# Optimization experiments

Hardware: AMD Instinct MI355X
Metric: run time of the kernel (lower is better)

The kernel has to match this reference:

```python
import jax, jax.numpy as jnp
import numpy as np

H = 256  # GRU hidden size
V = 56   # decoder vocab / fc1 out


def gru_cell(x, h, wih, whh, bih, bhh):
    # PyTorch GRU cell math (gate order: r, z, n)
    gi = x @ wih.T + bih
    gh = h @ whh.T + bhh
    ir, iz, inn = jnp.split(gi, 3, axis=-1)
    hr, hz, hn = jnp.split(gh, 3, axis=-1)
    r = jax.nn.sigmoid(ir + hr)
    z = jax.nn.sigmoid(iz + hz)
    n = jnp.tanh(inn + r * hn)
    return (1.0 - z) * n + z * h


def gru_scan(seq, h0, wih, whh, bih, bhh):
    def step(h, xt):
        h = gru_cell(xt, h, wih, whh, bih, bhh)
        return h, h
    hT, ys = jax.lax.scan(step, h0, seq)
    return ys, hT


def bigru(seq, pf, pb):
    # seq: (S, N, F). Returns (S, N, 2H), final fwd hidden (N,H), final bwd hidden (N,H)
    S, N, _ = seq.shape
    h0 = jnp.zeros((N, H), seq.dtype)
    yf, hf = gru_scan(seq, h0, *pf)
    yb_rev, hb = gru_scan(seq[::-1], h0, *pb)
    return jnp.concatenate([yf, yb_rev[::-1]], axis=-1), hf, hb


def setup_inputs() -> dict:
    key = jax.random.key(0)
    ks = iter(jax.random.split(key, 32))
    s = 0.05
    p = {}
    p["x"] = jax.random.normal(next(ks), (64, 48, 512, 2, 2), dtype=jnp.float32)
    # bi_gru_1: input 192
    for d in ("f", "b"):
        p[f"w_ih_1{d}"] = jax.random.normal(next(ks), (3 * H, 192), jnp.float32) * s
        p[f"w_hh_1{d}"] = jax.random.normal(next(ks), (3 * H, H), jnp.float32) * s
        p[f"b_ih_1{d}"] = jax.random.normal(next(ks), (3 * H,), jnp.float32) * s
        p[f"b_hh_1{d}"] = jax.random.normal(next(ks), (3 * H,), jnp.float32) * s
    # bi_gru_2: input 512
    for d in ("f", "b"):
        p[f"w_ih_2{d}"] = jax.random.normal(next(ks), (3 * H, 2 * H), jnp.float32) * s
        p[f"w_hh_2{d}"] = jax.random.normal(next(ks), (3 * H, H), jnp.float32) * s
        p[f"b_ih_2{d}"] = jax.random.normal(next(ks), (3 * H,), jnp.float32) * s
        p[f"b_hh_2{d}"] = jax.random.normal(next(ks), (3 * H,), jnp.float32) * s
    # decoder GRU: input 56
    p["w_ih_d"] = jax.random.normal(next(ks), (3 * H, V), jnp.float32) * s
    p["w_hh_d"] = jax.random.normal(next(ks), (3 * H, H), jnp.float32) * s
    p["b_ih_d"] = jax.random.normal(next(ks), (3 * H,), jnp.float32) * s
    p["b_hh_d"] = jax.random.normal(next(ks), (3 * H,), jnp.float32) * s
    p["w_fc1"] = jax.random.normal(next(ks), (V, H), jnp.float32) * s
    p["b_fc1"] = jax.random.normal(next(ks), (V,), jnp.float32) * s
    p["w_adj"] = jax.random.normal(next(ks), (H, 2 * H), jnp.float32) * s
    p["b_adj"] = jax.random.normal(next(ks), (H,), jnp.float32) * s
    p["target_length"] = 6
    return p


def reference(x,
              w_ih_1f, w_hh_1f, b_ih_1f, b_hh_1f,
              w_ih_1b, w_hh_1b, b_ih_1b, b_hh_1b,
              w_ih_2f, w_hh_2f, b_ih_2f, b_hh_2f,
              w_ih_2b, w_hh_2b, b_ih_2b, b_hh_2b,
              w_ih_d, w_hh_d, b_ih_d, b_hh_d,
              w_fc1, b_fc1, w_adj, b_adj,
              target_length):
    B, C, T, Hh, Ww = x.shape
    # permute(2,0,1,3,4).contiguous().view(B, T, -1): flat buffer in (T,B,..) order reshaped to (B,T,feat)
    seq = jnp.transpose(x, (2, 0, 1, 3, 4)).reshape(B, T, C * Hh * Ww)
    # GRUs run seq-first: seq dim = B, batch dim = T (faithful to the torch code)
    y1, _, _ = bigru(seq, (w_ih_1f, w_hh_1f, b_ih_1f, b_hh_1f),
                     (w_ih_1b, w_hh_1b, b_ih_1b, b_hh_1b))
    # dropout is identity at inference
    y2, hf, hb = bigru(y1, (w_ih_2f, w_hh_2f, b_ih_2f, b_hh_2f),
                       (w_ih_2b, w_hh_2b, b_ih_2b, b_hh_2b))
    combined = jnp.concatenate([hf, hb], axis=-1)       # (T, 2H)
    dec_h_all = combined @ w_adj.T + b_adj              # (T, H)
    dec_h = dec_h_all[:B]                               # loop over b in range(B) selects first B rows
    inp0 = jnp.zeros((B, V), x.dtype)

    def step(carry, _):
        inp, h = carry
        h = gru_cell(inp, h, w_ih_d, w_hh_d, b_ih_d, b_hh_d)
        out = h @ w_fc1.T + b_fc1
        return (out, h), out

    _, outs = jax.lax.scan(step, (inp0, dec_h), None, length=target_length)
    return jnp.transpose(outs, (1, 0, 2))  # (B, target_length, V)
```

## Files before the change

kernel.cpp:

```cpp
#include <hip/hip_runtime.h>
#include <hip/hip_fp16.h>
#include <stdint.h>


#define HD 256
#define G3 768
#define NSEQ 64
#define NSTEP 64

typedef _Float16 hvec2 __attribute__((ext_vector_type(2)));
typedef _Float16 f16x8 __attribute__((ext_vector_type(8)));
typedef float f32x4 __attribute__((ext_vector_type(4)));

__device__ __forceinline__ float sigmf(float x) {
    return 1.0f / (1.0f + __expf(-x));
}

#if __has_builtin(__builtin_amdgcn_fdot2)
__device__ __forceinline__ float fdot2u(uint32_t w, uint32_t h, float acc) {
    return __builtin_amdgcn_fdot2(__builtin_bit_cast(hvec2, w),
                                  __builtin_bit_cast(hvec2, h), acc, false);
}
#else
__device__ __forceinline__ float fdot2u(uint32_t w, uint32_t h, float acc) {
    const __half2 wv = __builtin_bit_cast(__half2, w);
    const __half2 hv = __builtin_bit_cast(__half2, h);
    acc += __half2float(wv.x) * __half2float(hv.x);
    acc += __half2float(wv.y) * __half2float(hv.y);
    return acc;
}
#endif

__device__ __forceinline__ uint32_t pkh(float a, float b) {
    uint32_t lo = __half_as_ushort(__float2half_rn(a));
    uint32_t hi = __half_as_ushort(__float2half_rn(b));
    return lo | (hi << 16);
}

#define L16(X) X(0) X(1) X(2) X(3) X(4) X(5) X(6) X(7) \
  X(8) X(9) X(10) X(11) X(12) X(13) X(14) X(15)

#define LRES(i) \
    const uint4 wr##i = wbase[(i) * G3]; \
    const uint4 wz##i = wbase[(i) * G3 + 256]; \
    const uint4 wn##i = wbase[(i) * G3 + 512];

#define DRES(i) { \
    const uint4 hp = *(const uint4*)&hb[hoff + 4 * (i)]; \
    ar0 = fdot2u(wr##i.x, hp.x, ar0); ar1 = fdot2u(wr##i.y, hp.y, ar1); \
    ar0 = fdot2u(wr##i.z, hp.z, ar0); ar1 = fdot2u(wr##i.w, hp.w, ar1); \
    az0 = fdot2u(wz##i.x, hp.x, az0); az1 = fdot2u(wz##i.y, hp.y, az1); \
    az0 = fdot2u(wz##i.z, hp.z, az0); az1 = fdot2u(wz##i.w, hp.w, az1); \
    an0 = fdot2u(wn##i.x, hp.x, an0); an1 = fdot2u(wn##i.y, hp.y, an1); \
    an0 = fdot2u(wn##i.z, hp.z, an0); an1 = fdot2u(wn##i.w, hp.w, an1); }

__global__ __launch_bounds__(256) void prep_all(
    const float* __restrict__ whh1f, const float* __restrict__ whh1b,
    const float* __restrict__ whh2f, const float* __restrict__ whh2b,
    const float* __restrict__ whhd,
    uint32_t* __restrict__ wt1f, uint32_t* __restrict__ wt1b,
    uint32_t* __restrict__ wt2f, uint32_t* __restrict__ wt2b,
    uint32_t* __restrict__ wtd,
    const float* __restrict__ wih1f, const float* __restrict__ wih1b,
    const float* __restrict__ wih2f, const float* __restrict__ wih2b,
    __half* __restrict__ wih1f_h, __half* __restrict__ wih1b_h,
    __half* __restrict__ wih2f_h, __half* __restrict__ wih2b_h,
    const float* __restrict__ wihd, const float* __restrict__ wadj,
    const float* __restrict__ wfc1,
    float* __restrict__ wihdT, float* __restrict__ wadjT,
    float* __restrict__ wfc1T,
    const float* __restrict__ x, __half* __restrict__ seqg)
{
    const int b   = blockIdx.x;
    const int tid = threadIdx.x;

    if (b < 480) {
        const int y = b / 96;
        const float* w; uint32_t* o;
        switch (y) {
            case 0: w = whh1f; o = wt1f; break;
            case 1: w = whh1b; o = wt1b; break;
            case 2: w = whh2f; o = wt2f; break;
            case 3: w = whh2b; o = wt2b; break;
            default: w = whhd; o = wtd; break;
        }
        const int idx = (b % 96) * 256 + tid;
        const int j = idx >> 5, q = idx & 31;
        const float4 fa = *(const float4*)(w + j * HD + 8 * q);
        const float4 fb = *(const float4*)(w + j * HD + 8 * q + 4);
        uint4 r;
        r.x = pkh(fa.x, fa.y); r.y = pkh(fa.z, fa.w);
        r.z = pkh(fb.x, fb.y); r.w = pkh(fb.z, fb.w);
        ((uint4*)o)[q * G3 + j] = r;
    } else if (b < 1536) {
        const float* s; __half* d; int i4;
        if (b < 624)       { s = wih1f; d = wih1f_h; i4 = (b - 480) * 256 + tid; }
        else if (b < 768)  { s = wih1b; d = wih1b_h; i4 = (b - 624) * 256 + tid; }
        else if (b < 1152) { s = wih2f; d = wih2f_h; i4 = (b - 768) * 256 + tid; }
        else               { s = wih2b; d = wih2b_h; i4 = (b - 1152) * 256 + tid; }
        const float4 v = *(const float4*)(s + (size_t)i4 * 4);
        __half2 lo; lo.x = __float2half_rn(v.x); lo.y = __float2half_rn(v.y);
        __half2 hi; hi.x = __float2half_rn(v.z); hi.y = __float2half_rn(v.w);
        *(__half2*)(d + (size_t)i4 * 4)     = lo;
        *(__half2*)(d + (size_t)i4 * 4 + 2) = hi;
    } else if (b < 2272) {
        const int idx = (b - 1536) * 256 + tid;
        if (idx < 43008) {
            int v = idx / G3, j = idx % G3;
            wihdT[idx] = wihd[j * 56 + v];
        } else if (idx < 43008 + 131072) {
            int i2 = idx - 43008;
            int f = i2 / HD, i = i2 % HD;
            wadjT[i2] = wadj[i * 512 + f];
        } else {
            int i3 = idx - 174080;
            int k = i3 / 56, v = i3 % 56;
            wfc1T[i3] = wfc1[v * HD + k];
        }
    } else {
        const int idx = (b - 2272) * 256 + tid;
        const int f = idx % 192;
        const int m = idx / 192;
        const int n = m >> 6, s = m & 63;
        seqg[idx] = __float2half(
            x[n * 98304 + (f >> 2) * 2048 + s * 32 + (f & 3)]);
    }
}

template <int K>
__global__ __launch_bounds__(256) void gemm_mfma(
    const __half* __restrict__ A,
    const __half* __restrict__ B0, const __half* __restrict__ B1,
    const float* __restrict__ bias0, const float* __restrict__ bias1,
    float* __restrict__ C0, float* __restrict__ C1)
{
    const __half* B    = blockIdx.z ? B1 : B0;
    const float*  bias = blockIdx.z ? bias1 : bias0;
    float*        C    = blockIdx.z ? C1 : C0;
    const int m0 = blockIdx.x * 64;
    const int n0 = blockIdx.y * 64;
    const int w  = threadIdx.x >> 6;
    const int l  = threadIdx.x & 63;
    const int lr = l & 15;
    const int lk = (l >> 4) * 8;

    const __half* arow = A + (size_t)(m0 + w * 16 + lr) * K + lk;
    const __half* brow = B + (size_t)(n0 + lr) * K + lk;

    f32x4 acc0 = {0.f, 0.f, 0.f, 0.f};
    f32x4 acc1 = acc0, acc2 = acc0, acc3 = acc0;

#pragma unroll
    for (int k0 = 0; k0 < K; k0 += 32) {
        const f16x8 a  = *(const f16x8*)(arow + k0);
        const f16x8 b0 = *(const f16x8*)(brow + k0);
        const f16x8 b1 = *(const f16x8*)(brow + 16 * K + k0);
        const f16x8 b2 = *(const f16x8*)(brow + 32 * K + k0);
        const f16x8 b3 = *(const f16x8*)(brow + 48 * K + k0);
        acc0 = __builtin_amdgcn_mfma_f32_16x16x32_f16(a, b0, acc0, 0, 0, 0);
        acc1 = __builtin_amdgcn_mfma_f32_16x16x32_f16(a, b1, acc1, 0, 0, 0);
        acc2 = __builtin_amdgcn_mfma_f32_16x16x32_f16(a, b2, acc2, 0, 0, 0);
        acc3 = __builtin_amdgcn_mfma_f32_16x16x32_f16(a, b3, acc3, 0, 0, 0);
    }

    const int crow = m0 + w * 16 + (l >> 4) * 4;
    const int ccol = n0 + lr;
    float* cp = C + (size_t)crow * G3 + ccol;
    const float bb0 = bias[ccol];
    const float bb1 = bias[ccol + 16];
    const float bb2 = bias[ccol + 32];
    const float bb3 = bias[ccol + 48];
#pragma unroll
    for (int j = 0; j < 4; ++j) {
        cp[(size_t)j * G3 +  0] = acc0[j] + bb0;
        cp[(size_t)j * G3 + 16] = acc1[j] + bb1;
        cp[(size_t)j * G3 + 32] = acc2[j] + bb2;
        cp[(size_t)j * G3 + 48] = acc3[j] + bb3;
    }
}

__global__ __launch_bounds__(512, 1) void gru_scan(
    const float* __restrict__ giF, const float* __restrict__ giB,
    const uint32_t* __restrict__ wTF, const uint32_t* __restrict__ wTB,
    const float* __restrict__ bhhF, const float* __restrict__ bhhB,
    __half* __restrict__ y1h, float* __restrict__ hfin)
{
    const int dir = blockIdx.x & 1;
    const int n   = blockIdx.x >> 1;
    const int t   = threadIdx.x;
    const int tr  = t & 255;
    const int kh  = t >> 8;
    const int hoff = kh * 64;
    const float* gi  = dir ? giB : giF;
    const float* bhh = dir ? bhhB : bhhF;
    const uint4* wbase = (const uint4*)(dir ? wTB : wTF)
                       + (size_t)(kh * 16) * G3 + tr;

    __shared__ __align__(16) uint32_t h1u[2][HD / 2];
    __shared__ float ph_r[HD], ph_z[HD], ph_n[HD];
    __shared__ float gin[2][G3];

    L16(LRES)
    const float bhr = bhh[tr], bhz = bhh[256 + tr], bhn = bhh[512 + tr];

    const float* gbase = gi + (size_t)n * NSTEP * G3;
    const int s0 = dir ? (NSTEP - 1) : 0;
#pragma unroll
    for (int i = t; i < G3; i += 512) gin[0][i] = gbase[s0 * G3 + i];

    float h_own = 0.0f;
    if (t < HD / 2) h1u[0][t] = 0u;
    __syncthreads();

    int s = s0;
    for (int step = 0; step < NSTEP; ++step) {
        const uint32_t* hb = h1u[step & 1];
        float ar0 = 0.f, ar1 = 0.f;
        float az0 = 0.f, az1 = 0.f;
        float an0 = 0.f, an1 = 0.f;
        L16(DRES)

        if (kh) {
            ph_r[tr] = ar0 + ar1;
            ph_z[tr] = az0 + az1;
            ph_n[tr] = an0 + an1;
        }
        __syncthreads();
        const int s_nxt = dir ? (step < NSTEP - 1 ? NSTEP - 2 - step : 0)
                              : (step < NSTEP - 1 ? step + 1 : NSTEP - 1);
        if (kh == 0) {
            const float* gcur = gin[step & 1];
            const float ghr = (ar0 + ar1) + ph_r[tr] + bhr;
            const float ghz = (az0 + az1) + ph_z[tr] + bhz;
            const float ghn = (an0 + an1) + ph_n[tr] + bhn;
            const float r  = sigmf(gcur[tr] + ghr);
            const float z  = sigmf(gcur[256 + tr] + ghz);
            const float nn = tanhf(gcur[512 + tr] + r * ghn);
            const float hnew = (1.0f - z) * nn + z * h_own;
            h_own = hnew;
            const __half hh = __float2half(hnew);
            ((__half*)h1u[(step + 1) & 1])[tr] = hh;
            y1h[(size_t)(n * NSTEP + s) * 512 + dir * HD + tr] = hh;
        } else {
            float* gnxt = gin[(step + 1) & 1];
            gnxt[tr]       = gbase[s_nxt * G3 + tr];
            gnxt[256 + tr] = gbase[s_nxt * G3 + 256 + tr];
            gnxt[512 + tr] = gbase[s_nxt * G3 + 512 + tr];
        }
        s = s_nxt;
        __syncthreads();
    }
    if (kh == 0)
        hfin[(size_t)(dir * NSEQ + n) * HD + tr] = h_own;
}

__global__ __launch_bounds__(768, 3) void decoder_kernel(
    const float* __restrict__ hfin, const float* __restrict__ wadjT,
    const float* __restrict__ badj, const uint32_t* __restrict__ wTd,
    const float* __restrict__ wihdT, const float* __restrict__ bihd,
    const float* __restrict__ bhhd, const float* __restrict__ wfc1T,
    const float* __restrict__ bfc1, float* __restrict__ out)
{
    const int n = blockIdx.x, t = threadIdx.x;
    const uint4* wq = (const uint4*)wTd + t;

    __shared__ __align__(16) uint32_t h1u[2][HD / 2];
    __shared__ float comb[512];
    __shared__ float ghs[G3], gis[G3];
    __shared__ float hfp[HD];
    __shared__ float inp[56];
    __shared__ float pf1[448];

    const float bi = bihd[t], bh = bhhd[t];

    if (t < 512)
        comb[t] = (t < 256) ? hfin[(size_t)n * HD + t]
                            : hfin[(size_t)(NSEQ + n) * HD + (t - 256)];
    if (t < 56) inp[t] = 0.0f;
    __syncthreads();

    float h_own = 0.0f;
    if (t < HD) {
        float acc = badj[t];
#pragma unroll 8
        for (int f = 0; f < 512; ++f) acc += wadjT[f * HD + t] * comb[f];
        h_own = acc;
        ((__half*)h1u[0])[t] = __float2half(acc);
        hfp[t] = acc;
    }
    __syncthreads();

    for (int step = 0; step < 6; ++step) {
        const uint32_t* hb = h1u[step & 1];
        float a0 = 0.f, a1 = 0.f;
#pragma unroll 8
        for (int q = 0; q < 32; ++q) {
            const uint4 w = wq[q * G3];
            const uint4 hp = *(const uint4*)&hb[4 * q];
            a0 = fdot2u(w.x, hp.x, a0); a1 = fdot2u(w.y, hp.y, a1);
            a0 = fdot2u(w.z, hp.z, a0); a1 = fdot2u(w.w, hp.w, a1);
        }
        float ai = bi;
#pragma unroll 8
        for (int v = 0; v < 56; ++v) ai += wihdT[v * G3 + t] * inp[v];
        ghs[t] = a0 + a1 + bh;
        gis[t] = ai;
        __syncthreads();
        if (t < HD) {
            const float r  = sigmf(gis[t] + ghs[t]);
            const float z  = sigmf(gis[HD + t] + ghs[HD + t]);
            const float nn = tanhf(gis[2 * HD + t] + r * ghs[2 * HD + t]);
            const float hnew = (1.0f - z) * nn + z * h_own;
            h_own = hnew;
            ((__half*)h1u[(step + 1) & 1])[t] = __float2half(hnew);
            hfp[t] = hnew;
        }
        __syncthreads();
        if (t < 448) {
            const int v = t >> 3, g = t & 7;
            float o = 0.f;
#pragma unroll
            for (int k2 = 0; k2 < 32; ++k2)
                o += wfc1T[(g * 32 + k2) * 56 + v] * hfp[g * 32 + k2];
            pf1[t] = o;
        }
        __syncthreads();
        if (t < 56) {
            float o = bfc1[t];
#pragma unroll
            for (int g = 0; g < 8; ++g) o += pf1[t * 8 + g];
            out[(size_t)n * 336 + step * 56 + t] = o;
            inp[t] = o;
        }
        __syncthreads();
    }
}

extern "C" void kernel_launch(void* const* d_in, const int* in_sizes, int n_in,
                              void* d_out, int out_size, void* d_ws, size_t ws_size,
                              hipStream_t stream)
{
    const float* x      = (const float*)d_in[0];
    const float* wih1f  = (const float*)d_in[1];
    const float* whh1f  = (const float*)d_in[2];
    const float* bih1f  = (const float*)d_in[3];
    const float* bhh1f  = (const float*)d_in[4];
    const float* wih1b  = (const float*)d_in[5];
    const float* whh1b  = (const float*)d_in[6];
    const float* bih1b  = (const float*)d_in[7];
    const float* bhh1b  = (const float*)d_in[8];
    const float* wih2f  = (const float*)d_in[9];
    const float* whh2f  = (const float*)d_in[10];
    const float* bih2f  = (const float*)d_in[11];
    const float* bhh2f  = (const float*)d_in[12];
    const float* wih2b  = (const float*)d_in[13];
    const float* whh2b  = (const float*)d_in[14];
    const float* bih2b  = (const float*)d_in[15];
    const float* bhh2b  = (const float*)d_in[16];
    const float* wihd   = (const float*)d_in[17];
    const float* whhd   = (const float*)d_in[18];
    const float* bihd   = (const float*)d_in[19];
    const float* bhhd   = (const float*)d_in[20];
    const float* wfc1   = (const float*)d_in[21];
    const float* bfc1   = (const float*)d_in[22];
    const float* wadj   = (const float*)d_in[23];
    const float* badj   = (const float*)d_in[24];

    float* ws = (float*)d_ws;
    __half*   seqg_h  = (__half*)(ws + 0);
    float*    gi_f    = ws + 393216;
    float*    gi_b    = ws + 3538944;
    __half*   y1h     = (__half*)(ws + 6684672);
    float*    hfin    = ws + 7733248;
    uint32_t* wt1f    = (uint32_t*)(ws + 7782400);
    uint32_t* wt1b    = (uint32_t*)(ws + 7880704);
    uint32_t* wt2f    = (uint32_t*)(ws + 7979008);
    uint32_t* wt2b    = (uint32_t*)(ws + 8077312);
    uint32_t* wtd     = (uint32_t*)(ws + 8175616);
    __half*   wih1f_h = (__half*)(ws + 8273920);
    __half*   wih1b_h = (__half*)(ws + 8347648);
    __half*   wih2f_h = (__half*)(ws + 8421376);
    __half*   wih2b_h = (__half*)(ws + 8617984);
    float*    wihdT   = ws + 8814592;
    float*    wadjT   = ws + 8857600;
    float*    wfc1T   = ws + 8988672;

    prep_all<<<5344, 256, 0, stream>>>(
        whh1f, whh1b, whh2f, whh2b, whhd,
        wt1f, wt1b, wt2f, wt2b, wtd,
        wih1f, wih1b, wih2f, wih2b,
        wih1f_h, wih1b_h, wih2f_h, wih2b_h,
        wihd, wadj, wfc1, wihdT, wadjT, wfc1T,
        x, seqg_h);

    gemm_mfma<192><<<dim3(64, 12, 2), 256, 0, stream>>>(
        seqg_h, wih1f_h, wih1b_h, bih1f, bih1b, gi_f, gi_b);
    gru_scan<<<128, 512, 0, stream>>>(
        gi_f, gi_b, wt1f, wt1b, bhh1f, bhh1b, y1h, hfin);

    gemm_mfma<512><<<dim3(64, 12, 2), 256, 0, stream>>>(
        y1h, wih2f_h, wih2b_h, bih2f, bih2b, gi_f, gi_b);
    gru_scan<<<128, 512, 0, stream>>>(
        gi_f, gi_b, wt2f, wt2b, bhh2f, bhh2b, y1h, hfin);

    decoder_kernel<<<64, 768, 0, stream>>>(
        hfin, wadjT, badj, wtd, wihdT, bihd, bhhd, wfc1T, bfc1,
        (float*)d_out);
}
```

Baseline: 345.6 us.

## Split GRU recurrent weights between registers and LDS; stage GEMM B tile in LDS

The scan kernel used to keep all 16 chunks of recurrent weights in registers per thread. It now keeps 10 chunks in registers and stages the other 6 in dynamic shared memory (about 147 KB), which lowers register pressure at the cost of LDS reads on every step. The input-projection GEMM now copies its 64-row B tile into padded shared memory before the MFMA loop, so B rows are no longer read repeatedly from global memory. Both changes add LDS traffic and a large LDS footprint per block.

Result: faster. 331.8 us (-4.0%).

```diff
diff --git a/kernel.cpp b/kernel.cpp
--- a/kernel.cpp
+++ b/kernel.cpp
@@ -7,6 +7,7 @@
 #define G3 768
 #define NSEQ 64
 #define NSTEP 64
+#define LSTG 6
 
 typedef _Float16 hvec2 __attribute__((ext_vector_type(2)));
 typedef _Float16 f16x8 __attribute__((ext_vector_type(8)));
@@ -37,8 +38,7 @@
     return lo | (hi << 16);
 }
 
-#define L16(X) X(0) X(1) X(2) X(3) X(4) X(5) X(6) X(7) \
-  X(8) X(9) X(10) X(11) X(12) X(13) X(14) X(15)
+#define L10(X) X(0) X(1) X(2) X(3) X(4) X(5) X(6) X(7) X(8) X(9)
 
 #define LRES(i) \
     const uint4 wr##i = wbase[(i) * G3]; \
@@ -134,6 +134,9 @@
     const float* __restrict__ bias0, const float* __restrict__ bias1,
     float* __restrict__ C0, float* __restrict__ C1)
 {
+    extern __shared__ __half Bs[];
+    constexpr int LDB = K + 8;
+
     const __half* B    = blockIdx.z ? B1 : B0;
     const float*  bias = blockIdx.z ? bias1 : bias0;
     float*        C    = blockIdx.z ? C1 : C0;
@@ -144,8 +147,16 @@
     const int lr = l & 15;
     const int lk = (l >> 4) * 8;
 
+    const __half* bsrc = B + (size_t)n0 * K;
+#pragma unroll
+    for (int i = threadIdx.x; i < 64 * K / 8; i += 256) {
+        const int r = i / (K / 8), g = i % (K / 8);
+        *(f16x8*)(Bs + r * LDB + g * 8) = *(const f16x8*)(bsrc + i * 8);
+    }
+    __syncthreads();
+
     const __half* arow = A + (size_t)(m0 + w * 16 + lr) * K + lk;
-    const __half* brow = B + (size_t)(n0 + lr) * K + lk;
+    const __half* brow = Bs + lr * LDB + lk;
 
     f32x4 acc0 = {0.f, 0.f, 0.f, 0.f};
     f32x4 acc1 = acc0, acc2 = acc0, acc3 = acc0;
@@ -154,9 +165,9 @@
     for (int k0 = 0; k0 < K; k0 += 32) {
         const f16x8 a  = *(const f16x8*)(arow + k0);
         const f16x8 b0 = *(const f16x8*)(brow + k0);
-        const f16x8 b1 = *(const f16x8*)(brow + 16 * K + k0);
-        const f16x8 b2 = *(const f16x8*)(brow + 32 * K + k0);
-        const f16x8 b3 = *(const f16x8*)(brow + 48 * K + k0);
+        const f16x8 b1 = *(const f16x8*)(brow + 16 * LDB + k0);
+        const f16x8 b2 = *(const f16x8*)(brow + 32 * LDB + k0);
+        const f16x8 b3 = *(const f16x8*)(brow + 48 * LDB + k0);
         acc0 = __builtin_amdgcn_mfma_f32_16x16x32_f16(a, b0, acc0, 0, 0, 0);
         acc1 = __builtin_amdgcn_mfma_f32_16x16x32_f16(a, b1, acc1, 0, 0, 0);
         acc2 = __builtin_amdgcn_mfma_f32_16x16x32_f16(a, b2, acc2, 0, 0, 0);
@@ -185,6 +196,8 @@
     const float* __restrict__ bhhF, const float* __restrict__ bhhB,
     __half* __restrict__ y1h, float* __restrict__ hfin)
 {
+    extern __shared__ __align__(16) uint4 wlds[];
+
     const int dir = blockIdx.x & 1;
     const int n   = blockIdx.x >> 1;
     const int t   = threadIdx.x;
@@ -200,7 +213,14 @@
     __shared__ float ph_r[HD], ph_z[HD], ph_n[HD];
     __shared__ float gin[2][G3];
 
-    L16(LRES)
+#pragma unroll
+    for (int c = 0; c < LSTG; ++c) {
+        wlds[((kh * LSTG + c) * 3 + 0) * 256 + tr] = wbase[(10 + c) * G3];
+        wlds[((kh * LSTG + c) * 3 + 1) * 256 + tr] = wbase[(10 + c) * G3 + 256];
+        wlds[((kh * LSTG + c) * 3 + 2) * 256 + tr] = wbase[(10 + c) * G3 + 512];
+    }
+
+    L10(LRES)
     const float bhr = bhh[tr], bhz = bhh[256 + tr], bhn = bhh[512 + tr];
 
     const float* gbase = gi + (size_t)n * NSTEP * G3;
@@ -218,7 +238,20 @@
         float ar0 = 0.f, ar1 = 0.f;
         float az0 = 0.f, az1 = 0.f;
         float an0 = 0.f, an1 = 0.f;
-        L16(DRES)
+        L10(DRES)
+#pragma unroll
+        for (int c = 0; c < LSTG; ++c) {
+            const uint4 hp = *(const uint4*)&hb[hoff + 4 * (10 + c)];
+            const uint4 wrl = wlds[((kh * LSTG + c) * 3 + 0) * 256 + tr];
+            const uint4 wzl = wlds[((kh * LSTG + c) * 3 + 1) * 256 + tr];
+            const uint4 wnl = wlds[((kh * LSTG + c) * 3 + 2) * 256 + tr];
+            ar0 = fdot2u(wrl.x, hp.x, ar0); ar1 = fdot2u(wrl.y, hp.y, ar1);
+            ar0 = fdot2u(wrl.z, hp.z, ar0); ar1 = fdot2u(wrl.w, hp.w, ar1);
+            az0 = fdot2u(wzl.x, hp.x, az0); az1 = fdot2u(wzl.y, hp.y, az1);
+            az0 = fdot2u(wzl.z, hp.z, az0); az1 = fdot2u(wzl.w, hp.w, az1);
+            an0 = fdot2u(wnl.x, hp.x, an0); an1 = fdot2u(wnl.y, hp.y, an1);
+            an0 = fdot2u(wnl.z, hp.z, an0); an1 = fdot2u(wnl.w, hp.w, an1);
+        }
 
         if (kh) {
             ph_r[tr] = ar0 + ar1;
@@ -385,6 +418,14 @@
     float*    wadjT   = ws + 8857600;
     float*    wfc1T   = ws + 8988672;
 
+    const int scan_lds = 2 * LSTG * 3 * 256 * 16;
+    hipFuncSetAttribute((const void*)gru_scan,
+                        hipFuncAttributeMaxDynamicSharedMemorySize, scan_lds);
+    const int g192_lds = 64 * (192 + 8) * 2;
+    const int g512_lds = 64 * (512 + 8) * 2;
+    hipFuncSetAttribute((const void*)gemm_mfma<512>,
+                        hipFuncAttributeMaxDynamicSharedMemorySize, g512_lds);
+
     prep_all<<<5344, 256, 0, stream>>>(
         whh1f, whh1b, whh2f, whh2b, whhd,
         wt1f, wt1b, wt2f, wt2b, wtd,
@@ -393,14 +434,14 @@
         wihd, wadj, wfc1, wihdT, wadjT, wfc1T,
         x, seqg_h);
 
-    gemm_mfma<192><<<dim3(64, 12, 2), 256, 0, stream>>>(
+    gemm_mfma<192><<<dim3(64, 12, 2), 256, g192_lds, stream>>>(
         seqg_h, wih1f_h, wih1b_h, bih1f, bih1b, gi_f, gi_b);
-    gru_scan<<<128, 512, 0, stream>>>(
+    gru_scan<<<128, 512, scan_lds, stream>>>(
         gi_f, gi_b, wt1f, wt1b, bhh1f, bhh1b, y1h, hfin);
 
-    gemm_mfma<512><<<dim3(64, 12, 2), 256, 0, stream>>>(
+    gemm_mfma<512><<<dim3(64, 12, 2), 256, g512_lds, stream>>>(
         y1h, wih2f_h, wih2b_h, bih2f, bih2b, gi_f, gi_b);
-    gru_scan<<<128, 512, 0, stream>>>(
+    gru_scan<<<128, 512, scan_lds, stream>>>(
         gi_f, gi_b, wt2f, wt2b, bhh2f, bhh2b, y1h, hfin);
 
     decoder_kernel<<<64, 768, 0, stream>>>(
```
